# Optimization experiments

Measured on AMD Instinct MI355X. Metric: run time of the kernel, lower is better.

The kernel has to match this reference:

```python
import jax, jax.numpy as jnp
import numpy as np

NUM_HEADS = 8
NUM_GROUPS = 32
EPS = 1e-5


def group_norm(x, gamma, beta):
    # x: [B, C, H, W]; normalize over (C//G, H, W) within each of G groups
    B, C, H, W = x.shape
    xg = x.reshape(B, NUM_GROUPS, C // NUM_GROUPS, H, W)
    mean = xg.mean(axis=(2, 3, 4), keepdims=True)
    var = xg.var(axis=(2, 3, 4), keepdims=True)
    xn = ((xg - mean) * jax.lax.rsqrt(var + EPS)).reshape(B, C, H, W)
    return xn * gamma[None, :, None, None] + beta[None, :, None, None]


def setup_inputs() -> dict:
    key = jax.random.key(0)
    ks = jax.random.split(key, 7)
    B, C, H, W = 16, 512, 32, 32
    x = jax.random.normal(ks[0], (B, C, H, W), dtype=jnp.float32)
    gamma = jnp.ones((C,), dtype=jnp.float32)
    beta = jnp.zeros((C,), dtype=jnp.float32)
    # 1x1 convs == per-pixel linear layers
    w_qkv = jax.random.normal(ks[1], (3 * C, C), dtype=jnp.float32) * (1.0 / np.sqrt(C))
    b_qkv = jax.random.normal(ks[2], (3 * C,), dtype=jnp.float32) * 0.02
    w_proj = jax.random.normal(ks[3], (C, C), dtype=jnp.float32) * (1.0 / np.sqrt(C))
    b_proj = jax.random.normal(ks[4], (C,), dtype=jnp.float32) * 0.02
    return {"x": x, "gamma": gamma, "beta": beta, "w_qkv": w_qkv,
            "b_qkv": b_qkv, "w_proj": w_proj, "b_proj": b_proj}


def reference(x, gamma, beta, w_qkv, b_qkv, w_proj, b_proj):
    B, C, H, W = x.shape
    nh = NUM_HEADS
    d = C // nh
    N = H * W
    h = group_norm(x, gamma, beta)
    # 1x1 conv: [B,C,H,W] x [3C,C] -> [B,3C,H,W]
    qkv = jnp.einsum('bchw,oc->bohw', h, w_qkv) + b_qkv[None, :, None, None]
    qkv = qkv.reshape(B, 3, nh, d, N)  # matches torch reshape(B,3,heads,d,HW)
    q, k, v = qkv[:, 0], qkv[:, 1], qkv[:, 2]
    scale = d ** (-0.5)
    attn = jnp.einsum('bhdn,bhdm->bhnm', q, k) * scale  # [B,h,N,N]
    attn = jax.nn.softmax(attn, axis=-1)
    out = jnp.einsum('bhnm,bhdm->bhdn', attn, v)  # [B,h,d,N]
    out = out.reshape(B, C, H, W)
    proj = jnp.einsum('bchw,oc->bohw', out, w_proj) + b_proj[None, :, None, None]
    return x + proj
```

## Files before the change

### kernel.cpp

```cpp
#include <hip/hip_runtime.h>
#include <cstddef>

#define B_  16
#define C_  512
#define N_  1024

typedef __attribute__((ext_vector_type(8))) __bf16 bf16x8;
typedef __attribute__((ext_vector_type(4))) float f32x4;
typedef __attribute__((ext_vector_type(4))) short s16x4;

__device__ __forceinline__ unsigned short f2bf(float x) {
  unsigned u = __float_as_uint(x);
  return (unsigned short)((u + 0x7fffu + ((u >> 16) & 1u)) >> 16);
}
__device__ __forceinline__ float bf2f(unsigned short h) {
  return __uint_as_float(((unsigned)h) << 16);
}

#define GLDS16(g, l)                                                            \
  __builtin_amdgcn_global_load_lds(                                             \
      (const __attribute__((address_space(1))) void*)(g),                       \
      (__attribute__((address_space(3))) void*)(l), 16, 0, 0)

__global__ __launch_bounds__(256) void wconv_kernel(
    const float* __restrict__ wq, const float* __restrict__ wp,
    unsigned short* __restrict__ oq, unsigned short* __restrict__ op) {
  int i = blockIdx.x * 256 + threadIdx.x;
  const float4* src; unsigned short* dst; int off;
  if (i < 196608) { src = (const float4*)wq; dst = oq; off = i; }
  else            { src = (const float4*)wp; dst = op; off = i - 196608; }
  float4 v = src[off];
  union { unsigned short s[4]; ushort4 u; } o;
  o.s[0] = f2bf(v.x); o.s[1] = f2bf(v.y);
  o.s[2] = f2bf(v.z); o.s[3] = f2bf(v.w);
  *(ushort4*)(dst + (size_t)off * 4) = o.u;
}

__global__ __launch_bounds__(256) void gn_kernel(
    const float* __restrict__ x, const float* __restrict__ gamma,
    const float* __restrict__ beta, unsigned short* __restrict__ hT) {
  int bg = blockIdx.x;
  int b = bg >> 5, g = bg & 31;
  size_t base = ((size_t)b * C_ + (size_t)g * 16) * N_;
  const float4* x4 = (const float4*)(x + base);
  int tid = threadIdx.x;

  float sum = 0.f, sq = 0.f;
  float4 vv[16];
#pragma unroll
  for (int i = 0; i < 16; i++) {
    float4 v = x4[tid + i * 256];
    vv[i] = v;
    sum += v.x + v.y + v.z + v.w;
    sq  += v.x * v.x + v.y * v.y + v.z * v.z + v.w * v.w;
  }
#pragma unroll
  for (int off = 32; off > 0; off >>= 1) {
    sum += __shfl_down(sum, off, 64);
    sq  += __shfl_down(sq, off, 64);
  }
  __shared__ float sm[4], sv[4];
  int lane = tid & 63, w = tid >> 6;
  if (lane == 0) { sm[w] = sum; sv[w] = sq; }
  __syncthreads();
  if (tid == 0) {
    float s = sm[0] + sm[1] + sm[2] + sm[3];
    float q = sv[0] + sv[1] + sv[2] + sv[3];
    float mean = s * (1.f / 16384.f);
    float var  = q * (1.f / 16384.f) - mean * mean;
    sm[0] = mean;
    sv[0] = rsqrtf(var + 1e-5f);
  }
  __syncthreads();
  float mean = sm[0], rstd = sv[0];

  union { unsigned short s[16]; uint4 u[2]; } row[4];
#pragma unroll
  for (int i = 0; i < 16; i++) {
    int c = g * 16 + i;
    float ga = gamma[c] * rstd;
    float be = beta[c] - mean * ga;
    float4 v = vv[i];
    row[0].s[i] = f2bf(v.x * ga + be);
    row[1].s[i] = f2bf(v.y * ga + be);
    row[2].s[i] = f2bf(v.z * ga + be);
    row[3].s[i] = f2bf(v.w * ga + be);
  }
#pragma unroll
  for (int j = 0; j < 4; j++) {
    uint4* dst = (uint4*)(hT + ((size_t)b * N_ + 4 * tid + j) * C_ + g * 16);
    dst[0] = row[j].u[0];
    dst[1] = row[j].u[1];
  }
}

template <int OUT_BF16>
__global__ __launch_bounds__(256) void gemm_mfma(
    const unsigned short* __restrict__ Wb, const float* __restrict__ bias,
    const unsigned short* __restrict__ InT, const float* __restrict__ resid,
    void* __restrict__ Out, int M) {
  __shared__ __align__(16) unsigned short As[128 * 32];
  __shared__ __align__(16) unsigned short Bs[128 * 32];

  const int b = blockIdx.z;
  const int n0 = blockIdx.x * 128, m0 = blockIdx.y * 128;
  const int tid = threadIdx.x;
  const int lane = tid & 63, wave = tid >> 6;
  const int col = lane & 15, quad = lane >> 4;
  const int wm = (wave >> 1) << 6, wn = (wave & 1) << 6;

  const unsigned short* Ag = Wb + (size_t)m0 * C_;
  const unsigned short* Bg = InT + ((size_t)b * N_ + n0) * C_;

  const int r0 = tid >> 2, c0 = (tid & 3) << 3;

  f32x4 acc[4][4];
#pragma unroll
  for (int i = 0; i < 4; i++)
#pragma unroll
    for (int j = 0; j < 4; j++) acc[i][j] = f32x4{0.f, 0.f, 0.f, 0.f};

  for (int k0 = 0; k0 < C_; k0 += 32) {
    __syncthreads();
    GLDS16(Ag + (size_t)r0 * C_ + k0 + c0,        &As[tid * 8]);
    GLDS16(Ag + (size_t)(r0 + 64) * C_ + k0 + c0, &As[(tid + 256) * 8]);
    GLDS16(Bg + (size_t)r0 * C_ + k0 + c0,        &Bs[tid * 8]);
    GLDS16(Bg + (size_t)(r0 + 64) * C_ + k0 + c0, &Bs[(tid + 256) * 8]);
    __syncthreads();

    bf16x8 af[4], bfr[4];
#pragma unroll
    for (int mt = 0; mt < 4; mt++)
      af[mt] = *(const bf16x8*)&As[(wm + mt * 16 + col) * 32 + quad * 8];
#pragma unroll
    for (int nt = 0; nt < 4; nt++)
      bfr[nt] = *(const bf16x8*)&Bs[(wn + nt * 16 + col) * 32 + quad * 8];
#pragma unroll
    for (int mt = 0; mt < 4; mt++)
#pragma unroll
      for (int nt = 0; nt < 4; nt++)
        acc[mt][nt] = __builtin_amdgcn_mfma_f32_16x16x32_bf16(
            af[mt], bfr[nt], acc[mt][nt], 0, 0, 0);
  }

#pragma unroll
  for (int mt = 0; mt < 4; mt++) {
    int mbase = m0 + wm + mt * 16 + quad * 4;
#pragma unroll
    for (int nt = 0; nt < 4; nt++) {
      int n = n0 + wn + nt * 16 + col;
#pragma unroll
      for (int r = 0; r < 4; r++) {
        int m = mbase + r;
        float v = acc[mt][nt][r] + bias[m];
        size_t off = ((size_t)b * M + m) * N_ + n;
        if constexpr (OUT_BF16) {
          ((unsigned short*)Out)[off] = f2bf(v);
        } else {
          ((float*)Out)[off] = v + resid[off];
        }
      }
    }
  }
}

__global__ __launch_bounds__(256) void attn_mfma(
    const unsigned short* __restrict__ qkv, unsigned short* __restrict__ aoT) {
  __shared__ __align__(16) unsigned short Kt[64 * 72];
  __shared__ __align__(16) unsigned short Vs[64 * 72];

  const int tid = threadIdx.x;
  const int wave = tid >> 6, lane = tid & 63;
  const int quad = lane >> 4, col = lane & 15;
  const int b = blockIdx.z, hh = blockIdx.y;
  const int qblk = blockIdx.x * 256 + wave * 64;

  const unsigned short* qp = qkv + ((size_t)b * 1536 + hh * 64) * N_;
  const unsigned short* kp = qp + (size_t)512 * N_;
  const unsigned short* vp = qp + (size_t)1024 * N_;

  bf16x8 qf[4][2];
#pragma unroll
  for (int nt = 0; nt < 4; nt++) {
    int qg = qblk + nt * 16 + col;
#pragma unroll
    for (int ks = 0; ks < 2; ks++) {
      union { unsigned short s[8]; bf16x8 v; } t;
#pragma unroll
      for (int j = 0; j < 8; j++) {
        int d = ks * 32 + quad * 8 + j;
        t.s[j] = f2bf(0.125f * bf2f(qp[(size_t)d * N_ + qg]));
      }
      qf[nt][ks] = t.v;
    }
  }

  float l_i[4];
  f32x4 O[4][4];
#pragma unroll
  for (int nt = 0; nt < 4; nt++) {
    l_i[nt] = 0.f;
#pragma unroll
    for (int mt = 0; mt < 4; mt++) O[mt][nt] = f32x4{0.f, 0.f, 0.f, 0.f};
  }

  const int sc = tid & 15, sd0 = tid >> 4;

  for (int kt = 0; kt < 16; kt++) {
    __syncthreads();
#pragma unroll
    for (int i = 0; i < 4; i++) {
      int d = sd0 + 16 * i;
      ushort4 kv = *(const ushort4*)(kp + (size_t)d * N_ + kt * 64 + sc * 4);
      ushort4 vv = *(const ushort4*)(vp + (size_t)d * N_ + kt * 64 + sc * 4);
      int sw = (sc >> 1) & 7;
      int dcol = (((d >> 3) ^ sw) << 3) | (d & 7);
      Kt[(4 * sc + 0) * 72 + dcol] = kv.x;
      Kt[(4 * sc + 1) * 72 + dcol] = kv.y;
      Kt[(4 * sc + 2) * 72 + dcol] = kv.z;
      Kt[(4 * sc + 3) * 72 + dcol] = kv.w;
      unsigned short* vrow = &Vs[d * 72 + 4 * sc];
      vrow[0] = vv.x; vrow[1] = vv.y;
      vrow[2] = vv.z; vrow[3] = vv.w;
    }
    __syncthreads();

    bf16x8 kf[4][2];
#pragma unroll
    for (int mt = 0; mt < 4; mt++) {
      int key = 16 * mt + col;
      int swr = (key >> 3) & 7;
#pragma unroll
      for (int ks = 0; ks < 2; ks++)
        kf[mt][ks] = *(const bf16x8*)&Kt[key * 72 + (((ks * 4 + quad) ^ swr) << 3)];
    }
    s16x4 vf[4][4];
#pragma unroll
    for (int mt = 0; mt < 4; mt++)
#pragma unroll
      for (int kc = 0; kc < 4; kc++)
        vf[mt][kc] = *(const s16x4*)&Vs[(16 * mt + col) * 72 + 16 * kc + quad * 4];

#pragma unroll
    for (int nt = 0; nt < 4; nt++) {
      f32x4 sf[4];
#pragma unroll
      for (int mt = 0; mt < 4; mt++) sf[mt] = f32x4{0.f, 0.f, 0.f, 0.f};
#pragma unroll
      for (int ks = 0; ks < 2; ks++)
#pragma unroll
        for (int mt = 0; mt < 4; mt++)
          sf[mt] = __builtin_amdgcn_mfma_f32_16x16x32_bf16(kf[mt][ks], qf[nt][ks], sf[mt], 0, 0, 0);

      s16x4 pb[4];
      float lsum = 0.f;
#pragma unroll
      for (int kc = 0; kc < 4; kc++) {
        float e0 = __expf(sf[kc][0]);
        float e1 = __expf(sf[kc][1]);
        float e2 = __expf(sf[kc][2]);
        float e3 = __expf(sf[kc][3]);
        lsum += (e0 + e1) + (e2 + e3);
        unsigned lo = __builtin_amdgcn_perm(__float_as_uint(e1), __float_as_uint(e0), 0x07060302u);
        unsigned hi = __builtin_amdgcn_perm(__float_as_uint(e3), __float_as_uint(e2), 0x07060302u);
        union { unsigned u[2]; s16x4 v; } t;
        t.u[0] = lo; t.u[1] = hi;
        pb[kc] = t.v;
      }
      l_i[nt] += lsum;

#pragma unroll
      for (int kc = 0; kc < 4; kc++)
#pragma unroll
        for (int mt = 0; mt < 4; mt++)
          O[mt][nt] = __builtin_amdgcn_mfma_f32_16x16x16bf16_1k(vf[mt][kc], pb[kc], O[mt][nt], 0, 0, 0);
    }
  }

#pragma unroll
  for (int nt = 0; nt < 4; nt++) {
    float ls = l_i[nt];
    ls += __shfl_xor(ls, 16, 64);
    ls += __shfl_xor(ls, 32, 64);
    float inv = 1.f / ls;
    int qg = qblk + nt * 16 + col;
    unsigned short* dst = aoT + ((size_t)b * N_ + qg) * C_ + hh * 64;
#pragma unroll
    for (int mt = 0; mt < 4; mt++) {
      union { unsigned short s[4]; ushort4 v; } o;
#pragma unroll
      for (int r = 0; r < 4; r++) o.s[r] = f2bf(O[mt][nt][r] * inv);
      *(ushort4*)(dst + mt * 16 + quad * 4) = o.v;
    }
  }
}

extern "C" void kernel_launch(void* const* d_in, const int* in_sizes, int n_in,
                              void* d_out, int out_size, void* d_ws, size_t ws_size,
                              hipStream_t stream) {
  (void)in_sizes; (void)n_in; (void)out_size; (void)ws_size;
  const float* x      = (const float*)d_in[0];
  const float* gamma  = (const float*)d_in[1];
  const float* beta   = (const float*)d_in[2];
  const float* w_qkv  = (const float*)d_in[3];
  const float* b_qkv  = (const float*)d_in[4];
  const float* w_proj = (const float*)d_in[5];
  const float* b_proj = (const float*)d_in[6];
  float* out = (float*)d_out;

  unsigned short* hT   = (unsigned short*)d_ws;
  unsigned short* qkvb = hT + (size_t)B_ * N_ * C_;
  unsigned short* aoT  = hT;
  unsigned short* wqb  = qkvb + (size_t)B_ * 1536 * N_;
  unsigned short* wpb  = wqb + (size_t)1536 * 512;

  wconv_kernel<<<dim3(1024), dim3(256), 0, stream>>>(w_qkv, w_proj, wqb, wpb);
  gn_kernel<<<dim3(B_ * 32), dim3(256), 0, stream>>>(x, gamma, beta, hT);
  gemm_mfma<1><<<dim3(8, 12, 16), dim3(256), 0, stream>>>(
      wqb, b_qkv, hT, (const float*)nullptr, (void*)qkvb, 1536);
  attn_mfma<<<dim3(4, 8, 16), dim3(256), 0, stream>>>(qkvb, aoT);
  gemm_mfma<0><<<dim3(8, 4, 16), dim3(256), 0, stream>>>(
      wpb, b_proj, aoT, x, (void*)out, 512);
}
```

Baseline: 225.7 us.

## Store K transposed in QKV conv epilogue and stream K/V from global

The QKV conv epilogue now writes the K slice transposed (token-major, 512 channels contiguous), so the attention kernel can load K fragments straight from global memory as 16-byte vectors. The attention kernel drops its shared-memory staging and both barriers per tile. It double-buffers K fragments in registers across tiles, raises MFMA priority with s_setprio, and sets launch bounds to two blocks per CU. The risks are higher register pressure and uncoalesced V loads from global that now depend on L1/L2 hit rates instead of LDS.

```diff
diff --git a/kernel.cpp b/kernel.cpp
--- a/kernel.cpp
+++ b/kernel.cpp
@@ -143,20 +143,36 @@
             af[mt], bfr[nt], acc[mt][nt], 0, 0, 0);
   }
 
+  const bool kT = OUT_BF16 && (m0 >= 512) && (m0 < 1024);
+
 #pragma unroll
   for (int mt = 0; mt < 4; mt++) {
     int mbase = m0 + wm + mt * 16 + quad * 4;
 #pragma unroll
     for (int nt = 0; nt < 4; nt++) {
       int n = n0 + wn + nt * 16 + col;
-#pragma unroll
-      for (int r = 0; r < 4; r++) {
-        int m = mbase + r;
-        float v = acc[mt][nt][r] + bias[m];
-        size_t off = ((size_t)b * M + m) * N_ + n;
-        if constexpr (OUT_BF16) {
-          ((unsigned short*)Out)[off] = f2bf(v);
+      if constexpr (OUT_BF16) {
+        if (kT) {
+          union { unsigned short s[4]; ushort4 v; } o;
+#pragma unroll
+          for (int r = 0; r < 4; r++)
+            o.s[r] = f2bf(acc[mt][nt][r] + bias[mbase + r]);
+          unsigned short* kt_out =
+              (unsigned short*)Out + ((size_t)b * 1536 + 512) * N_;
+          *(ushort4*)(kt_out + (size_t)n * 512 + (mbase - 512)) = o.v;
         } else {
+#pragma unroll
+          for (int r = 0; r < 4; r++) {
+            float v = acc[mt][nt][r] + bias[mbase + r];
+            ((unsigned short*)Out)[((size_t)b * M + mbase + r) * N_ + n] = f2bf(v);
+          }
+        }
+      } else {
+#pragma unroll
+        for (int r = 0; r < 4; r++) {
+          int m = mbase + r;
+          float v = acc[mt][nt][r] + bias[m];
+          size_t off = ((size_t)b * M + m) * N_ + n;
           ((float*)Out)[off] = v + resid[off];
         }
       }
@@ -164,20 +180,80 @@
   }
 }
 
-__global__ __launch_bounds__(256) void attn_mfma(
+
+__device__ __forceinline__ void load_k(bf16x8 (&kf)[4][2], const unsigned short* kb) {
+#pragma unroll
+  for (int mt = 0; mt < 4; mt++)
+#pragma unroll
+    for (int ks = 0; ks < 2; ks++)
+      kf[mt][ks] = *(const bf16x8*)(kb + mt * (16 * 512) + ks * 32);
+}
+
+__device__ __forceinline__ void load_v(s16x4 (&vf)[4][4], const unsigned short* vb) {
+#pragma unroll
+  for (int mt = 0; mt < 4; mt++)
+#pragma unroll
+    for (int kc = 0; kc < 4; kc++)
+      vf[mt][kc] = *(const s16x4*)(vb + mt * (16 * N_) + kc * 16);
+}
+
+__device__ __forceinline__ void attn_tile(const bf16x8 (&qf)[4][2],
+                                          const bf16x8 (&kf)[4][2],
+                                          const s16x4 (&vf)[4][4],
+                                          f32x4 (&O)[4][4], float (&l_i)[4]) {
+#pragma unroll
+  for (int nt = 0; nt < 4; nt++) {
+    f32x4 sf[4];
+#pragma unroll
+    for (int mt = 0; mt < 4; mt++) sf[mt] = f32x4{0.f, 0.f, 0.f, 0.f};
+    __builtin_amdgcn_s_setprio(1);
+#pragma unroll
+    for (int ks = 0; ks < 2; ks++)
+#pragma unroll
+      for (int mt = 0; mt < 4; mt++)
+        sf[mt] = __builtin_amdgcn_mfma_f32_16x16x32_bf16(
+            kf[mt][ks], qf[nt][ks], sf[mt], 0, 0, 0);
+    __builtin_amdgcn_s_setprio(0);
+
+    s16x4 pb[4];
+    float lsum = 0.f;
+#pragma unroll
+    for (int kc = 0; kc < 4; kc++) {
+      float e0 = __expf(sf[kc][0]);
+      float e1 = __expf(sf[kc][1]);
+      float e2 = __expf(sf[kc][2]);
+      float e3 = __expf(sf[kc][3]);
+      lsum += (e0 + e1) + (e2 + e3);
+      unsigned lo = __builtin_amdgcn_perm(__float_as_uint(e1), __float_as_uint(e0), 0x07060302u);
+      unsigned hi = __builtin_amdgcn_perm(__float_as_uint(e3), __float_as_uint(e2), 0x07060302u);
+      union { unsigned u[2]; s16x4 v; } t;
+      t.u[0] = lo; t.u[1] = hi;
+      pb[kc] = t.v;
+    }
+    l_i[nt] += lsum;
+
+    __builtin_amdgcn_s_setprio(1);
+#pragma unroll
+    for (int kc = 0; kc < 4; kc++)
+#pragma unroll
+      for (int mt = 0; mt < 4; mt++)
+        O[mt][nt] = __builtin_amdgcn_mfma_f32_16x16x16bf16_1k(
+            vf[mt][kc], pb[kc], O[mt][nt], 0, 0, 0);
+    __builtin_amdgcn_s_setprio(0);
+  }
+}
+
+__global__ __launch_bounds__(256, 2) void attn_mfma(
     const unsigned short* __restrict__ qkv, unsigned short* __restrict__ aoT) {
-  __shared__ __align__(16) unsigned short Kt[64 * 72];
-  __shared__ __align__(16) unsigned short Vs[64 * 72];
-
   const int tid = threadIdx.x;
   const int wave = tid >> 6, lane = tid & 63;
   const int quad = lane >> 4, col = lane & 15;
   const int b = blockIdx.z, hh = blockIdx.y;
   const int qblk = blockIdx.x * 256 + wave * 64;
 
-  const unsigned short* qp = qkv + ((size_t)b * 1536 + hh * 64) * N_;
-  const unsigned short* kp = qp + (size_t)512 * N_;
-  const unsigned short* vp = qp + (size_t)1024 * N_;
+  const unsigned short* qp  = qkv + ((size_t)b * 1536 + hh * 64) * N_;
+  const unsigned short* ktp = qkv + ((size_t)b * 1536 + 512) * N_ + hh * 64;
+  const unsigned short* vp  = qkv + ((size_t)b * 1536 + 1024 + hh * 64) * N_;
 
   bf16x8 qf[4][2];
 #pragma unroll
@@ -204,78 +280,27 @@
     for (int mt = 0; mt < 4; mt++) O[mt][nt] = f32x4{0.f, 0.f, 0.f, 0.f};
   }
 
-  const int sc = tid & 15, sd0 = tid >> 4;
-
-  for (int kt = 0; kt < 16; kt++) {
-    __syncthreads();
-#pragma unroll
-    for (int i = 0; i < 4; i++) {
-      int d = sd0 + 16 * i;
-      ushort4 kv = *(const ushort4*)(kp + (size_t)d * N_ + kt * 64 + sc * 4);
-      ushort4 vv = *(const ushort4*)(vp + (size_t)d * N_ + kt * 64 + sc * 4);
-      int sw = (sc >> 1) & 7;
-      int dcol = (((d >> 3) ^ sw) << 3) | (d & 7);
-      Kt[(4 * sc + 0) * 72 + dcol] = kv.x;
-      Kt[(4 * sc + 1) * 72 + dcol] = kv.y;
-      Kt[(4 * sc + 2) * 72 + dcol] = kv.z;
-      Kt[(4 * sc + 3) * 72 + dcol] = kv.w;
-      unsigned short* vrow = &Vs[d * 72 + 4 * sc];
-      vrow[0] = vv.x; vrow[1] = vv.y;
-      vrow[2] = vv.z; vrow[3] = vv.w;
-    }
-    __syncthreads();
-
-    bf16x8 kf[4][2];
-#pragma unroll
-    for (int mt = 0; mt < 4; mt++) {
-      int key = 16 * mt + col;
-      int swr = (key >> 3) & 7;
-#pragma unroll
-      for (int ks = 0; ks < 2; ks++)
-        kf[mt][ks] = *(const bf16x8*)&Kt[key * 72 + (((ks * 4 + quad) ^ swr) << 3)];
-    }
-    s16x4 vf[4][4];
-#pragma unroll
-    for (int mt = 0; mt < 4; mt++)
-#pragma unroll
-      for (int kc = 0; kc < 4; kc++)
-        vf[mt][kc] = *(const s16x4*)&Vs[(16 * mt + col) * 72 + 16 * kc + quad * 4];
-
-#pragma unroll
-    for (int nt = 0; nt < 4; nt++) {
-      f32x4 sf[4];
-#pragma unroll
-      for (int mt = 0; mt < 4; mt++) sf[mt] = f32x4{0.f, 0.f, 0.f, 0.f};
-#pragma unroll
-      for (int ks = 0; ks < 2; ks++)
-#pragma unroll
-        for (int mt = 0; mt < 4; mt++)
-          sf[mt] = __builtin_amdgcn_mfma_f32_16x16x32_bf16(kf[mt][ks], qf[nt][ks], sf[mt], 0, 0, 0);
-
-      s16x4 pb[4];
-      float lsum = 0.f;
-#pragma unroll
-      for (int kc = 0; kc < 4; kc++) {
-        float e0 = __expf(sf[kc][0]);
-        float e1 = __expf(sf[kc][1]);
-        float e2 = __expf(sf[kc][2]);
-        float e3 = __expf(sf[kc][3]);
-        lsum += (e0 + e1) + (e2 + e3);
-        unsigned lo = __builtin_amdgcn_perm(__float_as_uint(e1), __float_as_uint(e0), 0x07060302u);
-        unsigned hi = __builtin_amdgcn_perm(__float_as_uint(e3), __float_as_uint(e2), 0x07060302u);
-        union { unsigned u[2]; s16x4 v; } t;
-        t.u[0] = lo; t.u[1] = hi;
-        pb[kc] = t.v;
-      }
-      l_i[nt] += lsum;
-
-#pragma unroll
-      for (int kc = 0; kc < 4; kc++)
-#pragma unroll
-        for (int mt = 0; mt < 4; mt++)
-          O[mt][nt] = __builtin_amdgcn_mfma_f32_16x16x16bf16_1k(vf[mt][kc], pb[kc], O[mt][nt], 0, 0, 0);
-    }
-  }
+  const unsigned short* kb = ktp + (size_t)col * 512 + quad * 8;
+  const unsigned short* vb = vp + (size_t)col * N_ + quad * 4;
+
+  bf16x8 kA[4][2], kB[4][2];
+  s16x4 vf[4][4];
+  load_k(kA, kb);
+
+#pragma clang loop unroll(disable)
+  for (int kt = 0; kt < 14; kt += 2) {
+    load_v(vf, vb + kt * 64);
+    load_k(kB, kb + (size_t)(kt + 1) * (64 * 512));
+    attn_tile(qf, kA, vf, O, l_i);
+    load_v(vf, vb + (kt + 1) * 64);
+    load_k(kA, kb + (size_t)(kt + 2) * (64 * 512));
+    attn_tile(qf, kB, vf, O, l_i);
+  }
+  load_v(vf, vb + 14 * 64);
+  load_k(kB, kb + (size_t)15 * (64 * 512));
+  attn_tile(qf, kA, vf, O, l_i);
+  load_v(vf, vb + 15 * 64);
+  attn_tile(qf, kB, vf, O, l_i);
 
 #pragma unroll
   for (int nt = 0; nt < 4; nt++) {
```

Result: slower. 333.8 us (+47.9%).
